# Performance work log

Hardware: AMD Instinct MI355X
Metric: run time of the kernel (lower is better)

Reference implementation:

```python
import jax, jax.numpy as jnp
import numpy as np

# Dims: batch, queries, graph nodes, text len, hidden, heads, layers, ffn
B, NQ, NN, T, D, H, LAYERS, FF = 16, 32, 128, 352, 768, 8, 6, 3072
L = NQ + NN + T          # 512 total sequence length
HD = D // H              # 96 head dim
NEG = -1e9               # additive mask value (HF uses dtype min; -1e9 is equivalent post-softmax)
LN_EPS = 1e-12           # BERT LayerNorm eps


def _ln(x, g, b):
    m = x.mean(-1, keepdims=True)
    v = ((x - m) ** 2).mean(-1, keepdims=True)
    return (x - m) * jax.lax.rsqrt(v + LN_EPS) * g + b


def setup_inputs() -> dict:
    key = jax.random.key(0)
    ks = iter(jax.random.split(key, 32))

    def nrm(shape, s=0.02):
        return jax.random.normal(next(ks), shape, jnp.float32) * s

    return {
        "graph_node_features": jax.random.normal(next(ks), (B, NN, D), jnp.float32),
        "text_embeds": jax.random.normal(next(ks), (B, T, D), jnp.float32),
        "text_atts": jnp.ones((B, T), jnp.int32),
        "graph_mask": jnp.ones((B, NN), jnp.int32),
        "query_tokens": nrm((1, NQ, D), 1.0),   # nn.Parameter(torch.randn(...))
        "gproj_w": nrm((D, D)), "gproj_b": jnp.zeros((D,)),
        "pos_emb": nrm((L, D)), "tok_emb": nrm((D,)),  # token_type row 0
        "emb_ln_g": jnp.ones((D,)), "emb_ln_b": jnp.zeros((D,)),
        "qkv_w": nrm((LAYERS, D, 3 * D)), "qkv_b": jnp.zeros((LAYERS, 3 * D)),
        "ao_w": nrm((LAYERS, D, D)), "ao_b": jnp.zeros((LAYERS, D)),
        "ln1_g": jnp.ones((LAYERS, D)), "ln1_b": jnp.zeros((LAYERS, D)),
        "ff1_w": nrm((LAYERS, D, FF)), "ff1_b": jnp.zeros((LAYERS, FF)),
        "ff2_w": nrm((LAYERS, FF, D)), "ff2_b": jnp.zeros((LAYERS, D)),
        "ln2_g": jnp.ones((LAYERS, D)), "ln2_b": jnp.zeros((LAYERS, D)),
    }


def _itg_bias(text_atts, graph_mask):
    # Build the custom ITG prefix-LM mask: bidirectional over [queries|graph],
    # causal over text, and queries/graph blocked from attending to text.
    keep = jnp.concatenate(
        [jnp.ones((B, NQ), jnp.int32), graph_mask, text_atts], axis=1)  # [B, L]
    ts = NQ + NN
    idx = jnp.arange(L)
    is_text = idx >= ts
    pair = (keep[:, :, None] * keep[:, None, :]).astype(bool)          # padding mask
    causal_ok = jnp.where(is_text[:, None] & is_text[None, :],
                          idx[:, None] >= idx[None, :], True)           # tril in text block
    block_ok = ~((~is_text)[:, None] & is_text[None, :])                # prefix cannot see text
    mask = pair & causal_ok & block_ok                                  # [B, L, L]
    return jnp.where(mask, 0.0, NEG)[:, None, :, :]                     # [B, 1, L, L]


def reference(graph_node_features, text_embeds, text_atts, graph_mask,
              query_tokens, gproj_w, gproj_b, pos_emb, tok_emb,
              emb_ln_g, emb_ln_b, qkv_w, qkv_b, ao_w, ao_b,
              ln1_g, ln1_b, ff1_w, ff1_b, ff2_w, ff2_b, ln2_g, ln2_b):
    gfeat = graph_node_features @ gproj_w + gproj_b
    qtok = jnp.broadcast_to(query_tokens, (B, NQ, D))
    x = jnp.concatenate([qtok, gfeat, text_embeds], axis=1)             # [B, L, D]
    bias = _itg_bias(text_atts, graph_mask)

    # BERT embeddings (inputs_embeds path): + position + token_type(0), LN (dropout off)
    x = _ln(x + pos_emb[None] + tok_emb, emb_ln_g, emb_ln_b)

    scale = 1.0 / np.sqrt(HD)
    for i in range(LAYERS):
        qkv = x @ qkv_w[i] + qkv_b[i]
        q, k, v = jnp.split(qkv, 3, axis=-1)
        q = q.reshape(B, L, H, HD)
        k = k.reshape(B, L, H, HD)
        v = v.reshape(B, L, H, HD)
        s = jnp.einsum('bqhd,bkhd->bhqk', q, k) * scale + bias
        p = jax.nn.softmax(s, axis=-1)
        ctx = jnp.einsum('bhqk,bkhd->bqhd', p, v).reshape(B, L, D)
        x = _ln(x + ctx @ ao_w[i] + ao_b[i], ln1_g[i], ln1_b[i])
        h = jax.nn.gelu(x @ ff1_w[i] + ff1_b[i], approximate=False)
        x = _ln(x + h @ ff2_w[i] + ff2_b[i], ln2_g[i], ln2_b[i])

    return x[:, NQ + NN:, :]   # text_feats [B, T, D]
```

## Files before the change

### kernel.cpp

```cpp
#include <hip/hip_runtime.h>
#include <math.h>

typedef __bf16 bf16;
typedef __bf16 bf16x8 __attribute__((ext_vector_type(8)));
typedef float f32x4 __attribute__((ext_vector_type(4)));

#define NQ   32
#define NN_  128
#define TT   352
#define DD   768
#define NH   8
#define HDIM 96
#define LSEQ 512
#define TSPLIT 160
#define FFD  3072
#define NLAYER 6
#define NBATCH 16

#define GLOAD(srcp, dstp)                                                     \
    __builtin_amdgcn_global_load_lds(                                         \
        (const __attribute__((address_space(1))) void*)(srcp),                \
        (__attribute__((address_space(3))) void*)(dstp), 16, 0, 0)

template <int ACT>
__global__ __launch_bounds__(256) void gemm_bt(
    const bf16* __restrict__ A, const bf16* __restrict__ Bt,
    bf16* __restrict__ C, const float* __restrict__ bias,
    int K, int lda, int ldb, int ldc, float alpha, int Nstore)
{
    __shared__ __attribute__((aligned(16))) bf16 As[2 * 128 * 32];
    __shared__ __attribute__((aligned(16))) bf16 Bs[2 * 128 * 32];

    const int n0 = blockIdx.x * 128, m0 = blockIdx.y * 128;
    const int t = threadIdx.x;
    const int w = t >> 6, l = t & 63;
    const int wm = w >> 1, wn = w & 1;
    const int lr = l & 15, quad = l >> 4;

    f32x4 acc[4][4] = {};

    const int f0 = w * 1024 + l * 8;
    const int ra0 = f0 >> 5, ca0 = f0 & 31;
    const int ra1 = (f0 + 512) >> 5, ca1 = (f0 + 512) & 31;
    const bf16* a0 = A  + (size_t)(m0 + ra0) * lda + ca0;
    const bf16* a1 = A  + (size_t)(m0 + ra1) * lda + ca1;
    const bf16* b0 = Bt + (size_t)(n0 + ra0) * ldb + ca0;
    const bf16* b1 = Bt + (size_t)(n0 + ra1) * ldb + ca1;

    const int nt = K >> 5;

    {
        bf16* pA = &As[w * 1024];
        bf16* pB = &Bs[w * 1024];
        GLOAD(a0, pA);
        GLOAD(a1, pA + 512);
        GLOAD(b0, pB);
        GLOAD(b1, pB + 512);
    }

    for (int tt = 0; tt < nt; ++tt) {
        __syncthreads();
        const int cur = (tt & 1) << 12;
        const int nxt = 4096 - cur;
        if (tt + 1 < nt) {
            const int k0 = (tt + 1) << 5;
            bf16* pA = &As[nxt + w * 1024];
            bf16* pB = &Bs[nxt + w * 1024];
            GLOAD(a0 + k0, pA);
            GLOAD(a1 + k0, pA + 512);
            GLOAD(b0 + k0, pB);
            GLOAD(b1 + k0, pB + 512);
        }

        bf16x8 af[4], bf_[4];
#pragma unroll
        for (int i = 0; i < 4; ++i)
            af[i] = *(const bf16x8*)&As[cur + (wm * 64 + i * 16 + lr) * 32 + quad * 8];
#pragma unroll
        for (int j = 0; j < 4; ++j)
            bf_[j] = *(const bf16x8*)&Bs[cur + (wn * 64 + j * 16 + lr) * 32 + quad * 8];
#pragma unroll
        for (int i = 0; i < 4; ++i)
#pragma unroll
            for (int j = 0; j < 4; ++j)
                acc[i][j] = __builtin_amdgcn_mfma_f32_16x16x32_bf16(af[i], bf_[j], acc[i][j], 0, 0, 0);
    }

#pragma unroll
    for (int i = 0; i < 4; ++i) {
        const int grow = m0 + wm * 64 + i * 16 + quad * 4;
#pragma unroll
        for (int j = 0; j < 4; ++j) {
            const int gcol = n0 + wn * 64 + j * 16 + lr;
            if (gcol >= Nstore) continue;
            float bv = bias ? bias[gcol] : 0.0f;
#pragma unroll
            for (int r = 0; r < 4; ++r) {
                float v = acc[i][j][r] * alpha + bv;
                if (ACT == 1) v = 0.5f * v * (1.0f + erff(v * 0.70710678118654752f));
                C[(size_t)(grow + r) * ldc + gcol] = (bf16)v;
            }
        }
    }
}

__global__ __launch_bounds__(256) void flash_attn(
    const bf16* __restrict__ qkv, bf16* __restrict__ ctx,
    const int* __restrict__ tatts, const int* __restrict__ gmask)
{
    __shared__ __attribute__((aligned(16))) bf16 Qs[64 * 104];
    __shared__ __attribute__((aligned(16))) bf16 Ks[64 * 104];
    __shared__ __attribute__((aligned(16))) bf16 Vs[96 * 72];
    __shared__ __attribute__((aligned(16))) bf16 Ps[64 * 72];
    __shared__ int keep[512];

    const int qt = blockIdx.x;
    const int bh = blockIdx.y;
    const int b = bh >> 3, h = bh & 7;
    const int q0 = qt * 64;
    const int t = threadIdx.x;
    const int w = t >> 6, l = t & 63;
    const int lr = l & 15, quad = l >> 4;
    const float scale = 0.10206207261596577f;

    const bf16* qbase = qkv + (size_t)b * 512 * 2304 + h * 96;
    const bf16* kbase = qbase + 768;
    const bf16* vbase = qbase + 1536;

    for (int j = t; j < 512; j += 256)
        keep[j] = (j < NQ) ? 1 : (j < TSPLIT ? gmask[b * NN_ + j - NQ]
                                             : tatts[b * TT + j - TSPLIT]);

#pragma unroll
    for (int c = 0; c < 3; ++c) {
        const int idx = t * 8 + c * 2048;
        const int r = idx / 96, d = idx % 96;
        *(bf16x8*)&Qs[r * 104 + d] =
            *(const bf16x8*)&qbase[(size_t)(q0 + r) * 2304 + d];
    }
    __syncthreads();

    int ki[4];
    int ig[4];
#pragma unroll
    for (int r = 0; r < 4; ++r) {
        ig[r] = q0 + w * 16 + quad * 4 + r;
        ki[r] = keep[ig[r]];
    }

    float m_run[4] = {-1e30f, -1e30f, -1e30f, -1e30f};
    float l_run[4] = {0.f, 0.f, 0.f, 0.f};
    f32x4 oc[6] = {};

    const int JMAX = (qt < 3) ? 128 : q0;
    for (int j0 = 0; j0 <= JMAX; j0 += 64) {
        __syncthreads();
#pragma unroll
        for (int c = 0; c < 3; ++c) {
            const int idx = t * 8 + c * 2048;
            const int r = idx / 96, d = idx % 96;
            *(bf16x8*)&Ks[r * 104 + d] =
                *(const bf16x8*)&kbase[(size_t)(j0 + r) * 2304 + d];
            bf16x8 vv = *(const bf16x8*)&vbase[(size_t)(j0 + r) * 2304 + d];
#pragma unroll
            for (int jj = 0; jj < 8; ++jj)
                Vs[(d + jj) * 72 + r] = vv[jj];
        }
        __syncthreads();

        bf16x8 aq[3];
#pragma unroll
        for (int ds = 0; ds < 3; ++ds)
            aq[ds] = *(const bf16x8*)&Qs[(w * 16 + lr) * 104 + ds * 32 + quad * 8];
        f32x4 sc[4];
#pragma unroll
        for (int cb = 0; cb < 4; ++cb) {
            f32x4 a = {};
#pragma unroll
            for (int ds = 0; ds < 3; ++ds) {
                bf16x8 bk = *(const bf16x8*)&Ks[(cb * 16 + lr) * 104 + ds * 32 + quad * 8];
                a = __builtin_amdgcn_mfma_f32_16x16x32_bf16(aq[ds], bk, a, 0, 0, 0);
            }
            sc[cb] = a;
        }

        float tm[4] = {-1e30f, -1e30f, -1e30f, -1e30f};
#pragma unroll
        for (int cb = 0; cb < 4; ++cb) {
            const int jg = j0 + cb * 16 + lr;
            const int kj = keep[jg];
#pragma unroll
            for (int r = 0; r < 4; ++r) {
                const int i = ig[r];
                bool ok = ki[r] && kj;
                if (i < TSPLIT && jg >= TSPLIT) ok = false;
                if (i >= TSPLIT && jg >= TSPLIT && i < jg) ok = false;
                float s = sc[cb][r] * scale + (ok ? 0.f : -1e9f);
                sc[cb][r] = s;
                tm[r] = fmaxf(tm[r], s);
            }
        }
#pragma unroll
        for (int off = 1; off < 16; off <<= 1)
#pragma unroll
            for (int r = 0; r < 4; ++r)
                tm[r] = fmaxf(tm[r], __shfl_xor(tm[r], off));

        float alpha_[4], ts[4] = {0.f, 0.f, 0.f, 0.f};
#pragma unroll
        for (int r = 0; r < 4; ++r) {
            const float mn = fmaxf(m_run[r], tm[r]);
            alpha_[r] = __expf(m_run[r] - mn);
            m_run[r] = mn;
            l_run[r] *= alpha_[r];
        }
#pragma unroll
        for (int db = 0; db < 6; ++db)
#pragma unroll
            for (int r = 0; r < 4; ++r)
                oc[db][r] *= alpha_[r];

#pragma unroll
        for (int cb = 0; cb < 4; ++cb)
#pragma unroll
            for (int r = 0; r < 4; ++r) {
                const float p = __expf(sc[cb][r] - m_run[r]);
                ts[r] += p;
                Ps[(w * 16 + quad * 4 + r) * 72 + cb * 16 + lr] = (bf16)p;
            }
#pragma unroll
        for (int off = 1; off < 16; off <<= 1)
#pragma unroll
            for (int r = 0; r < 4; ++r)
                ts[r] += __shfl_xor(ts[r], off);
#pragma unroll
        for (int r = 0; r < 4; ++r) l_run[r] += ts[r];

        __syncthreads();

#pragma unroll
        for (int l0 = 0; l0 < 64; l0 += 32) {
            bf16x8 ap = *(const bf16x8*)&Ps[(w * 16 + lr) * 72 + l0 + quad * 8];
#pragma unroll
            for (int db = 0; db < 6; ++db) {
                bf16x8 bv = *(const bf16x8*)&Vs[(db * 16 + lr) * 72 + l0 + quad * 8];
                oc[db] = __builtin_amdgcn_mfma_f32_16x16x32_bf16(ap, bv, oc[db], 0, 0, 0);
            }
        }
    }

#pragma unroll
    for (int r = 0; r < 4; ++r) {
        const float inv = 1.f / l_run[r];
        bf16* orow = ctx + ((size_t)b * 512 + ig[r]) * 768 + h * 96;
#pragma unroll
        for (int db = 0; db < 6; ++db)
            orow[db * 16 + lr] = (bf16)(oc[db][r] * inv);
    }
}

__global__ void transpose_w(const float* __restrict__ in, bf16* __restrict__ out,
                            int R, int C)
{
    __shared__ bf16 tile[32][33];
    const int c0 = blockIdx.x * 32, r0 = blockIdx.y * 32;
    const int tx = threadIdx.x & 31, ty = threadIdx.x >> 5;
    for (int i = ty; i < 32; i += 8)
        tile[i][tx] = (bf16)in[(size_t)(r0 + i) * C + c0 + tx];
    __syncthreads();
    for (int i = ty; i < 32; i += 8)
        out[(size_t)(c0 + i) * R + r0 + tx] = tile[tx][i];
}

__global__ void cvt_bf16(const float* __restrict__ in, bf16* __restrict__ out, int n)
{
    const int idx = blockIdx.x * 256 + threadIdx.x;
    if (idx < n) out[idx] = (bf16)in[idx];
}

__device__ __forceinline__ void block_reduce_2(float& a, float& b)
{
#pragma unroll
    for (int off = 32; off; off >>= 1) {
        a += __shfl_xor(a, off);
        b += __shfl_xor(b, off);
    }
    __shared__ float sa[4], sb[4];
    const int w = threadIdx.x >> 6;
    if ((threadIdx.x & 63) == 0) { sa[w] = a; sb[w] = b; }
    __syncthreads();
    a = sa[0] + sa[1] + sa[2] + sa[3];
    b = sb[0] + sb[1] + sb[2] + sb[3];
}

__global__ void embed_ln(const float* __restrict__ qtok, const bf16* __restrict__ gfeat,
                         const float* __restrict__ text, const float* __restrict__ pos,
                         const float* __restrict__ tok, const float* __restrict__ g,
                         const float* __restrict__ bb, bf16* __restrict__ x)
{
    const int row = blockIdx.x;
    const int l = row & 511, b = row >> 9;
    const int t = threadIdx.x;

    float vals[3], s = 0.f, sq = 0.f;
#pragma unroll
    for (int c = 0; c < 3; ++c) {
        const int d = t + c * 256;
        float base;
        if (l < NQ)           base = qtok[(size_t)l * DD + d];
        else if (l < TSPLIT)  base = (float)gfeat[((size_t)b * NN_ + (l - NQ)) * DD + d];
        else                  base = text[((size_t)b * TT + (l - TSPLIT)) * DD + d];
        float v = base + pos[(size_t)l * DD + d] + tok[d];
        vals[c] = v; s += v; sq += v * v;
    }
    block_reduce_2(s, sq);
    const float mean = s * (1.f / 768.f);
    const float var = sq * (1.f / 768.f) - mean * mean;
    const float rs = rsqrtf(var + 1e-12f);
    bf16* o = x + (size_t)row * DD;
#pragma unroll
    for (int c = 0; c < 3; ++c) {
        const int d = t + c * 256;
        o[d] = (bf16)((vals[c] - mean) * rs * g[d] + bb[d]);
    }
}

__global__ void ln_rows(const bf16* __restrict__ X, const bf16* __restrict__ Y,
                        bf16* __restrict__ Out, const float* __restrict__ g,
                        const float* __restrict__ bb)
{
    const int row = blockIdx.x;
    const int t = threadIdx.x;
    const bf16* xr = X + (size_t)row * DD;
    const bf16* yr = Y + (size_t)row * DD;
    float vals[3], s = 0.f, sq = 0.f;
#pragma unroll
    for (int c = 0; c < 3; ++c) {
        const int d = t + c * 256;
        float v = (float)xr[d] + (float)yr[d];
        vals[c] = v; s += v; sq += v * v;
    }
    block_reduce_2(s, sq);
    const float mean = s * (1.f / 768.f);
    const float var = sq * (1.f / 768.f) - mean * mean;
    const float rs = rsqrtf(var + 1e-12f);
    bf16* o = Out + (size_t)row * DD;
#pragma unroll
    for (int c = 0; c < 3; ++c) {
        const int d = t + c * 256;
        o[d] = (bf16)((vals[c] - mean) * rs * g[d] + bb[d]);
    }
}

__global__ void copy_out(const bf16* __restrict__ x, float* __restrict__ out)
{
    const size_t idx = (size_t)blockIdx.x * 256 + threadIdx.x;
    const int d = idx % DD;
    const size_t row = idx / DD;
    const int t = row % TT;
    const int b = row / TT;
    out[idx] = (float)x[((size_t)b * LSEQ + TSPLIT + t) * DD + d];
}

static void launch_gemm(const bf16* A, const bf16* Bt, bf16* C, const float* bias,
                        int M, int K, int lda, int ldb, int ldc,
                        float alpha, int Nstore, int act, hipStream_t stream)
{
    dim3 grid((Nstore + 127) / 128, M / 128, 1);
    if (act)
        gemm_bt<1><<<grid, 256, 0, stream>>>(A, Bt, C, bias, K, lda, ldb, ldc, alpha, Nstore);
    else
        gemm_bt<0><<<grid, 256, 0, stream>>>(A, Bt, C, bias, K, lda, ldb, ldc, alpha, Nstore);
}

extern "C" void kernel_launch(void* const* d_in, const int* in_sizes, int n_in,
                              void* d_out, int out_size, void* d_ws, size_t ws_size,
                              hipStream_t stream)
{
    const float* gnf     = (const float*)d_in[0];
    const float* text    = (const float*)d_in[1];
    const int*   tatts   = (const int*)d_in[2];
    const int*   gmask   = (const int*)d_in[3];
    const float* qtok    = (const float*)d_in[4];
    const float* gproj_w = (const float*)d_in[5];
    const float* gproj_b = (const float*)d_in[6];
    const float* pos     = (const float*)d_in[7];
    const float* tok     = (const float*)d_in[8];
    const float* eg      = (const float*)d_in[9];
    const float* eb      = (const float*)d_in[10];
    const float* qkv_w   = (const float*)d_in[11];
    const float* qkv_b   = (const float*)d_in[12];
    const float* ao_w    = (const float*)d_in[13];
    const float* ao_b    = (const float*)d_in[14];
    const float* ln1g    = (const float*)d_in[15];
    const float* ln1b    = (const float*)d_in[16];
    const float* ff1_w   = (const float*)d_in[17];
    const float* ff1_b   = (const float*)d_in[18];
    const float* ff2_w   = (const float*)d_in[19];
    const float* ff2_b   = (const float*)d_in[20];
    const float* ln2g    = (const float*)d_in[21];
    const float* ln2b    = (const float*)d_in[22];
    float* out = (float*)d_out;

    bf16* ws   = (bf16*)d_ws;
    bf16* wt1  = ws;
    bf16* wt2  = wt1 + 2359296;
    bf16* x    = wt2 + 2359296;
    bf16* ctx  = x   + 6291456;
    bf16* t1   = ctx + 6291456;
    bf16* u    = t1  + 6291456;
    bf16* qkvb = u;
    bf16* hbuf = u;
    bf16* gfeat = t1;
    bf16* gnfb  = u;

    dim3 blk(256);

    cvt_bf16<<<6144, blk, 0, stream>>>(gnf, gnfb, 1572864);
    transpose_w<<<dim3(24, 24), blk, 0, stream>>>(gproj_w, wt1, 768, 768);
    launch_gemm(gnfb, wt1, gfeat, gproj_b, 2048, 768, 768, 768, 768,
                1.f, 768, 0, stream);
    embed_ln<<<8192, blk, 0, stream>>>(qtok, gfeat, text, pos, tok, eg, eb, x);

    for (int i = 0; i < NLAYER; ++i) {
        transpose_w<<<dim3(72, 24), blk, 0, stream>>>(
            qkv_w + (size_t)i * 768 * 2304, wt1, 768, 2304);
        launch_gemm(x, wt1, qkvb, qkv_b + i * 2304,
                    8192, 768, 768, 768, 2304, 1.f, 2304, 0, stream);
        flash_attn<<<dim3(8, 128), blk, 0, stream>>>(qkvb, ctx, tatts, gmask);
        transpose_w<<<dim3(24, 24), blk, 0, stream>>>(
            ao_w + (size_t)i * 589824, wt1, 768, 768);
        launch_gemm(ctx, wt1, t1, ao_b + i * 768,
                    8192, 768, 768, 768, 768, 1.f, 768, 0, stream);
        ln_rows<<<8192, blk, 0, stream>>>(x, t1, x, ln1g + i * 768, ln1b + i * 768);

        transpose_w<<<dim3(96, 24), blk, 0, stream>>>(
            ff1_w + (size_t)i * 2359296, wt1, 768, 3072);
        transpose_w<<<dim3(24, 96), blk, 0, stream>>>(
            ff2_w + (size_t)i * 2359296, wt2, 3072, 768);
        launch_gemm(x, wt1, hbuf, ff1_b + i * 3072,
                    8192, 768, 768, 768, 3072, 1.f, 3072, 1, stream);
        launch_gemm(hbuf, wt2, t1, ff2_b + i * 768,
                    8192, 3072, 3072, 3072, 768, 1.f, 768, 0, stream);
        ln_rows<<<8192, blk, 0, stream>>>(x, t1, x, ln2g + i * 768, ln2b + i * 768);
    }

    copy_out<<<16896, blk, 0, stream>>>(x, out);

    (void)in_sizes; (void)n_in; (void)out_size; (void)ws_size;
}
```

Baseline: 2.208 ms.

## Triple-buffer GEMM LDS tiles with two-stage prefetch and explicit vmcnt waits

The bf16 GEMM main loop moves from double buffering to three LDS buffers, prefetching two K-tiles ahead. Explicit s_waitcnt vmcnt plus a raw s_barrier replace __syncthreads, so the loads for the next tile can stay in flight while the current tile is computed. This is meant to hide global-to-LDS latency. The cost is 50% more shared memory per block, which may reduce occupancy. The hand-placed waitcnt and barrier ordering also has to be exactly right to avoid races.

```diff
diff --git a/kernel.cpp b/kernel.cpp
--- a/kernel.cpp
+++ b/kernel.cpp
@@ -28,8 +28,8 @@
     bf16* __restrict__ C, const float* __restrict__ bias,
     int K, int lda, int ldb, int ldc, float alpha, int Nstore)
 {
-    __shared__ __attribute__((aligned(16))) bf16 As[2 * 128 * 32];
-    __shared__ __attribute__((aligned(16))) bf16 Bs[2 * 128 * 32];
+    __shared__ __attribute__((aligned(16))) bf16 As[3 * 4096];
+    __shared__ __attribute__((aligned(16))) bf16 Bs[3 * 4096];
 
     const int n0 = blockIdx.x * 128, m0 = blockIdx.y * 128;
     const int t = threadIdx.x;
@@ -52,26 +52,33 @@
     {
         bf16* pA = &As[w * 1024];
         bf16* pB = &Bs[w * 1024];
-        GLOAD(a0, pA);
-        GLOAD(a1, pA + 512);
-        GLOAD(b0, pB);
-        GLOAD(b1, pB + 512);
-    }
-
-    for (int tt = 0; tt < nt; ++tt) {
-        __syncthreads();
-        const int cur = (tt & 1) << 12;
-        const int nxt = 4096 - cur;
-        if (tt + 1 < nt) {
-            const int k0 = (tt + 1) << 5;
-            bf16* pA = &As[nxt + w * 1024];
-            bf16* pB = &Bs[nxt + w * 1024];
-            GLOAD(a0 + k0, pA);
-            GLOAD(a1 + k0, pA + 512);
-            GLOAD(b0 + k0, pB);
-            GLOAD(b1 + k0, pB + 512);
-        }
-
+        GLOAD(a0, pA);        GLOAD(a1, pA + 512);
+        GLOAD(b0, pB);        GLOAD(b1, pB + 512);
+        pA += 4096;  pB += 4096;
+        GLOAD(a0 + 32, pA);   GLOAD(a1 + 32, pA + 512);
+        GLOAD(b0 + 32, pB);   GLOAD(b1 + 32, pB + 512);
+    }
+
+    int cb = 0;
+    int wb = 2;
+    for (int T = 0; T < nt; ++T) {
+        if (T == nt - 1) {
+            asm volatile("s_waitcnt vmcnt(0)" ::: "memory");
+        } else {
+            asm volatile("s_waitcnt vmcnt(4)" ::: "memory");
+        }
+        __builtin_amdgcn_s_barrier();
+        __builtin_amdgcn_sched_barrier(0);
+
+        if (T + 2 < nt) {
+            const int k0 = (T + 2) << 5;
+            bf16* pA = &As[wb * 4096 + w * 1024];
+            bf16* pB = &Bs[wb * 4096 + w * 1024];
+            GLOAD(a0 + k0, pA);   GLOAD(a1 + k0, pA + 512);
+            GLOAD(b0 + k0, pB);   GLOAD(b1 + k0, pB + 512);
+        }
+
+        const int cur = cb << 12;
         bf16x8 af[4], bf_[4];
 #pragma unroll
         for (int i = 0; i < 4; ++i)
@@ -84,6 +91,9 @@
 #pragma unroll
             for (int j = 0; j < 4; ++j)
                 acc[i][j] = __builtin_amdgcn_mfma_f32_16x16x32_bf16(af[i], bf_[j], acc[i][j], 0, 0, 0);
+
+        cb = (cb == 2) ? 0 : cb + 1;
+        wb = (wb == 2) ? 0 : wb + 1;
     }
 
 #pragma unroll
```

After: 2.180 ms. No clear change (-1.3%).
